# Performance work log

Hardware: AMD Instinct MI355X
Metric: run time of the kernel (lower is better)

## Reference

```python
import jax, jax.numpy as jnp
import numpy as np

D_MODEL, HEAD_DIM = 1024, 128

def setup_inputs() -> dict:
    key = jax.random.key(0)
    kx, kq, kk, kv = jax.random.split(key, 4)
    x = jax.random.normal(kx, (4, 4096, D_MODEL), dtype=jnp.float32)
    s = 1.0 / np.sqrt(D_MODEL)
    Wq = jax.random.normal(kq, (D_MODEL, HEAD_DIM), dtype=jnp.float32) * s
    Wk = jax.random.normal(kk, (D_MODEL, HEAD_DIM), dtype=jnp.float32) * s
    Wv = jax.random.normal(kv, (D_MODEL, HEAD_DIM), dtype=jnp.float32) * s
    return {"x": x, "Wq": Wq, "Wk": Wk, "Wv": Wv}

def reference(x, Wq, Wk, Wv):
    # x: [b, s, d_model]; Wq/Wk/Wv: [d_model, head_dim]
    q = jnp.einsum('bsd,dh->bsh', x, Wq)
    k = jnp.einsum('bsd,dh->bsh', x, Wk)
    v = jnp.einsum('bsd,dh->bsh', x, Wv)
    seq = x.shape[1]
    scale = 1.0 / jnp.sqrt(jnp.asarray(q.shape[-1], q.dtype))
    scores = jnp.einsum('bqh,bkh->bqk', q, k) * scale  # [b, s, s]
    causal = jnp.tril(jnp.ones((seq, seq), dtype=bool))
    scores = jnp.where(causal, scores, jnp.asarray(-jnp.inf, scores.dtype))
    attn = jax.nn.softmax(scores, axis=-1)
    return jnp.einsum('bqk,bkh->bqh', attn, v)
```

## Files before the change

kernel.cpp:

```cpp
#include <hip/hip_runtime.h>
#include <hip/hip_bf16.h>
#include <math.h>

#define D_MODEL 1024
#define HD 128
#define SEQ 4096

typedef __bf16 bf16x8 __attribute__((ext_vector_type(8)));
typedef float f32x4 __attribute__((ext_vector_type(4)));
typedef unsigned int u32;
typedef u32 u32x4 __attribute__((ext_vector_type(4)));

__device__ __forceinline__ unsigned short f2bf(float f) {
    union { float f; u32 u; } c; c.f = f;
    u32 u = c.u;
    u = (u + 0x7fffu + ((u >> 16) & 1u)) >> 16;
    return (unsigned short)u;
}
__device__ __forceinline__ u32 pk2(float a, float b) {
    __hip_bfloat162 h = __float22bfloat162_rn(make_float2(a, b));
    union { __hip_bfloat162 h; u32 u; } c; c.h = h; return c.u;
}
__device__ __forceinline__ void dma16(void* lds, const void* g) {
    __builtin_amdgcn_global_load_lds(
        (const __attribute__((address_space(1))) u32*)g,
        (__attribute__((address_space(3))) u32*)lds, 16, 0, 0);
}
__device__ __forceinline__ void drain_dma()  { __builtin_amdgcn_s_waitcnt(0x0F70); }
__device__ __forceinline__ void drain_dma4() { __builtin_amdgcn_s_waitcnt(0x0F74); }

__global__ __launch_bounds__(256)
void wt_kernel(const float* __restrict__ Wq, const float* __restrict__ Wk,
               const float* __restrict__ Wv, unsigned short* __restrict__ Wt) {
    __shared__ float wsf[64][129];
    const int t = threadIdx.x;
    const int k0 = blockIdx.x * 64;
    const int mat = blockIdx.y;
    const float* W = (mat == 0) ? Wq : (mat == 1) ? Wk : Wv;
    const float sc = (mat == 0) ? (0.08838834764831845f * 1.4426950408889634f) : 1.0f;
    {
        const int r = t >> 2, c = (t & 3) * 32;
        const float* src = W + (size_t)(k0 + r) * HD + c;
        #pragma unroll
        for (int j = 0; j < 32; j += 4)
            *reinterpret_cast<f32x4*>(&wsf[r][c + j]) = *reinterpret_cast<const f32x4*>(src + j);
    }
    __syncthreads();
    const int n = t >> 1, ks = (t & 1) * 32;
    u32 ow[16];
    #pragma unroll
    for (int j = 0; j < 16; ++j)
        ow[j] = pk2(wsf[ks + 2 * j][n] * sc, wsf[ks + 2 * j + 1][n] * sc);
    unsigned short* dst = Wt + (size_t)(mat * HD + n) * D_MODEL + k0 + ks;
    #pragma unroll
    for (int j = 0; j < 4; ++j)
        *reinterpret_cast<u32x4*>(dst + j * 8) = (u32x4){ow[4*j], ow[4*j+1], ow[4*j+2], ow[4*j+3]};
}

__global__ __launch_bounds__(256)
void proj_kernel(const float* __restrict__ x, const unsigned short* __restrict__ Wt,
                 unsigned short* __restrict__ Qb, unsigned short* __restrict__ Kb,
                 unsigned short* __restrict__ Vt) {
    __shared__ __align__(1024) char ps[49152];
    const int t = threadIdx.x;
    const int w = t >> 6, l = t & 63, li = l & 15, g2 = l >> 4;
    const int id = blockIdx.x;
    const int grp = id / 24, win = id % 24;
    const int nbase = (win >> 3) * 128;
    const int rowbase = (grp * 8 + (win & 7)) * 64;

    f32x4 acc[8];
    #pragma unroll
    for (int nt = 0; nt < 8; ++nt) acc[nt] = (f32x4){0.f, 0.f, 0.f, 0.f};

    const int lrow = l >> 3;
    const int xg = (l & 7) ^ (lrow & 6);
    const int wgr = (l & 7) ^ lrow;
    const int wrow_add = (wgr >> 2) << 6;
    const int wkc = (wgr & 3) * 8;

    auto stage = [&](int k0, int buf) {
        #pragma unroll
        for (int j = 0; j < 2; ++j) {
            int r0 = w * 16 + 8 * j;
            dma16(ps + buf * 8192 + r0 * 128,
                  x + (size_t)(rowbase + r0 + lrow) * D_MODEL + k0 + xg * 4);
            dma16(ps + 24576 + buf * 8192 + r0 * 128,
                  Wt + (size_t)(nbase + r0 + lrow + wrow_add) * D_MODEL + k0 + wkc);
        }
    };

    stage(0, 0);
    stage(32, 1);
    for (int it = 0; it < 32; ++it) {
        const int buf = it % 3;
        if (it < 31) drain_dma4(); else drain_dma();
        __syncthreads();
        if (it + 2 < 32) stage((it + 2) * 32, (it + 2) % 3);
        const char* xb = ps + buf * 8192 + (w * 16 + li) * 128 + (((2 * g2) ^ (li & 6)) * 16);
        f32x4 x0 = *reinterpret_cast<const f32x4*>(xb);
        f32x4 x1 = *reinterpret_cast<const f32x4*>(xb + 16);
        union { u32 d[4]; bf16x8 v; } cva;
        cva.d[0] = pk2(x0[0], x0[1]); cva.d[1] = pk2(x0[2], x0[3]);
        cva.d[2] = pk2(x1[0], x1[1]); cva.d[3] = pk2(x1[2], x1[3]);
        bf16x8 af = cva.v;
        #pragma unroll
        for (int nt = 0; nt < 8; ++nt) {
            bf16x8 bfr = *reinterpret_cast<const bf16x8*>(
                ps + 24576 + buf * 8192 + ((nt & 3) * 16 + li) * 128 +
                ((((nt >> 2) * 4 + g2) ^ (li & 7)) * 16));
            acc[nt] = __builtin_amdgcn_mfma_f32_16x16x32_bf16(af, bfr, acc[nt], 0, 0, 0);
        }
    }

    if (nbase < 256) {
        unsigned short* P = nbase ? Kb : Qb;
        #pragma unroll
        for (int nt = 0; nt < 8; ++nt)
            #pragma unroll
            for (int r = 0; r < 4; ++r) {
                int grow = rowbase + w * 16 + g2 * 4 + r;
                P[(size_t)grow * HD + nt * 16 + li] = f2bf(acc[nt][r]);
            }
    } else {
        int grow0 = rowbase + w * 16 + g2 * 4;
        int b_ = grow0 >> 12, s_ = grow0 & 4095;
        #pragma unroll
        for (int nt = 0; nt < 8; ++nt) {
            ushort4 s4;
            s4.x = f2bf(acc[nt][0]); s4.y = f2bf(acc[nt][1]);
            s4.z = f2bf(acc[nt][2]); s4.w = f2bf(acc[nt][3]);
            *reinterpret_cast<ushort4*>(&Vt[((size_t)b_ * HD + nt * 16 + li) * SEQ + s_]) = s4;
        }
    }
}

__global__ __launch_bounds__(256, 2)
void attn_kernel(const unsigned short* __restrict__ Qb, const unsigned short* __restrict__ Kb,
                 const unsigned short* __restrict__ Vt, float* __restrict__ outO,
                 unsigned short* __restrict__ Obf, float* __restrict__ Lbuf) {
    __shared__ __align__(1024) char smem[73728];
    const int t = threadIdx.x;
    const int w = t >> 6, l = t & 63, li = l & 15, g2 = l >> 4;
    const int qh = w >> 1, kh = w & 1;
    const int b = blockIdx.x & 3;
    const int u = blockIdx.x >> 2;
    const int g = 63 - (u >> 2);
    const int c = u & 3;
    const int R = g + 1;
    const int ts = (c * R) >> 2, te = ((c + 1) * R) >> 2;
    const int q0 = g * 64;
    const size_t rowb = (size_t)b * SEQ;
    const int koff = kh * 32;

    const unsigned short* KbB = Kb + rowb * HD;
    const unsigned short* VtB = Vt + (size_t)b * HD * SEQ;
    const int vgran = ((l & 7) ^ (l >> 3)) * 8;

    auto stage = [&](int it, char* base) {
        const int j0 = it * 64;
        #pragma unroll
        for (int j = 0; j < 4; ++j) {
            int rK = w * 16 + 4 * j + (l >> 4);
            dma16(base + (w * 16 + 4 * j) * 256,
                  KbB + (size_t)(j0 + rK) * 128 + (((l & 15) ^ (rK & 7)) * 8));
            int rV = w * 32 + 8 * j + (l >> 3);
            dma16(base + 16384 + (w * 32 + 8 * j) * 128,
                  VtB + (size_t)rV * SEQ + j0 + vgran);
        }
    };

    bf16x8 qf[2][4];
    #pragma unroll
    for (int qt = 0; qt < 2; ++qt)
        #pragma unroll
        for (int ks = 0; ks < 4; ++ks)
            qf[qt][ks] = *reinterpret_cast<const bf16x8*>(
                Qb + (rowb + q0 + qh * 32 + qt * 16 + li) * HD + ks * 32 + g2 * 8);

    f32x4 acco[2][8];
    #pragma unroll
    for (int qt = 0; qt < 2; ++qt)
        #pragma unroll
        for (int dt = 0; dt < 8; ++dt) acco[qt][dt] = (f32x4){0.f, 0.f, 0.f, 0.f};
    float ls[2] = {0.f, 0.f};

    const int gV = ((4 * kh + g2) ^ (li & 7)) * 16;

    if (ts < te) stage(ts, smem);
    for (int it = ts; it < te; ++it) {
        char* cbuf = smem + ((it - ts) & 1) * 32768;
        char* nbuf = smem + (((it - ts) & 1) ^ 1) * 32768;
        drain_dma();
        __syncthreads();
        if (it + 1 < te) stage(it + 1, nbuf);

        f32x4 accs[2][2];
        #pragma unroll
        for (int qt = 0; qt < 2; ++qt)
            #pragma unroll
            for (int kt = 0; kt < 2; ++kt) accs[qt][kt] = (f32x4){0.f, 0.f, 0.f, 0.f};
        #pragma unroll
        for (int kt = 0; kt < 2; ++kt) {
            const char* kb = cbuf + (koff + kt * 16 + li) * 256;
            #pragma unroll
            for (int ks = 0; ks < 4; ++ks) {
                bf16x8 kf = *reinterpret_cast<const bf16x8*>(kb + (((4 * ks + g2) ^ (li & 7)) * 16));
                accs[0][kt] = __builtin_amdgcn_mfma_f32_16x16x32_bf16(kf, qf[0][ks], accs[0][kt], 0, 0, 0);
                accs[1][kt] = __builtin_amdgcn_mfma_f32_16x16x32_bf16(kf, qf[1][ks], accs[1][kt], 0, 0, 0);
            }
        }

        const bool masked = (it == g);
        #pragma unroll
        for (int qt = 0; qt < 2; ++qt) {
            const int prow = qh * 32 + qt * 16 + li;
            #pragma unroll
            for (int kt = 0; kt < 2; ++kt) {
                float p[4];
                #pragma unroll
                for (int r = 0; r < 4; ++r) {
                    float s = accs[qt][kt][r];
                    if (masked && (koff + kt * 16 + g2 * 4 + r > prow)) s = -INFINITY;
                    p[r] = __builtin_amdgcn_exp2f(s - 16.0f);
                    ls[qt] += p[r];
                }
                union { u32 d[2]; uint2 v; } pw;
                pw.d[0] = pk2(p[0], p[1]); pw.d[1] = pk2(p[2], p[3]);
                int gr = (kh * 4 + kt * 2 + (g2 >> 1)) ^ (prow & 7);
                *reinterpret_cast<uint2*>(
                    smem + 65536 + prow * 128 + gr * 16 + (g2 & 1) * 8) = pw.v;
            }
        }

        bf16x8 pb[2];
        #pragma unroll
        for (int qt = 0; qt < 2; ++qt) {
            const int prow = qh * 32 + qt * 16 + li;
            pb[qt] = *reinterpret_cast<const bf16x8*>(
                smem + 65536 + prow * 128 + (((kh * 4 + g2) ^ (prow & 7)) * 16));
        }
        #pragma unroll
        for (int dt = 0; dt < 8; ++dt) {
            bf16x8 va = *reinterpret_cast<const bf16x8*>(cbuf + 16384 + (dt * 16 + li) * 128 + gV);
            acco[0][dt] = __builtin_amdgcn_mfma_f32_16x16x32_bf16(va, pb[0], acco[0][dt], 0, 0, 0);
            acco[1][dt] = __builtin_amdgcn_mfma_f32_16x16x32_bf16(va, pb[1], acco[1][dt], 0, 0, 0);
        }
    }

    #pragma unroll
    for (int qt = 0; qt < 2; ++qt) {
        ls[qt] += __shfl_xor(ls[qt], 16);
        ls[qt] += __shfl_xor(ls[qt], 32);
    }

    float (*Osum)[132] = (float(*)[132])smem;
    float* Lsh = (float*)(smem + 33792);
    __syncthreads();
    if (l < 16) {
        Lsh[kh * 64 + qh * 32 + l]      = ls[0];
        Lsh[kh * 64 + qh * 32 + 16 + l] = ls[1];
    }
    if (kh == 0) {
        #pragma unroll
        for (int qt = 0; qt < 2; ++qt)
            #pragma unroll
            for (int dt = 0; dt < 8; ++dt)
                *reinterpret_cast<f32x4*>(
                    &Osum[qh * 32 + qt * 16 + li][dt * 16 + g2 * 4]) = acco[qt][dt];
    }
    __syncthreads();
    if (kh == 1) {
        #pragma unroll
        for (int qt = 0; qt < 2; ++qt)
            #pragma unroll
            for (int dt = 0; dt < 8; ++dt) {
                f32x4* p = reinterpret_cast<f32x4*>(
                    &Osum[qh * 32 + qt * 16 + li][dt * 16 + g2 * 4]);
                f32x4 v = *p;
                #pragma unroll
                for (int j = 0; j < 4; ++j) v[j] += acco[qt][dt][j];
                *p = v;
            }
    }
    __syncthreads();

    if (t < 64)
        Lbuf[(size_t)c * 16384 + rowb + q0 + t] = Lsh[t] + Lsh[64 + t];
    #pragma unroll
    for (int k = 0; k < 8; ++k) {
        int idx = t + k * 256;
        int row = idx >> 5, col = (idx & 31) * 4;
        f32x4 o = *reinterpret_cast<const f32x4*>(&Osum[row][col]);
        size_t grow = rowb + q0 + row;
        if (c == 3) {
            *reinterpret_cast<f32x4*>(&outO[grow * HD + col]) = o;
        } else {
            union { u32 d[2]; uint2 v; } pkd;
            pkd.d[0] = pk2(o[0], o[1]); pkd.d[1] = pk2(o[2], o[3]);
            *reinterpret_cast<uint2*>(&Obf[(size_t)c * 2097152 + grow * HD + col]) = pkd.v;
        }
    }
}

__global__ __launch_bounds__(256)
void merge_kernel(float* __restrict__ outO, const unsigned short* __restrict__ Obf,
                  const float* __restrict__ Lbuf) {
    int tid = blockIdx.x * 256 + threadIdx.x;
    #pragma unroll
    for (int k = 0; k < 4; ++k) {
        int idx = tid + k * 131072;
        int row = idx >> 5, col = (idx & 31) * 4;
        float lsum = Lbuf[row] + Lbuf[16384 + row] + Lbuf[32768 + row] + Lbuf[49152 + row];
        float inv = 1.f / lsum;
        f32x4 o = *reinterpret_cast<const f32x4*>(&outO[(size_t)row * HD + col]);
        #pragma unroll
        for (int cc = 0; cc < 3; ++cc) {
            ushort4 uu = *reinterpret_cast<const ushort4*>(
                &Obf[(size_t)cc * 2097152 + (size_t)row * HD + col]);
            union { u32 u; float f; } a, b2, c2, d2;
            a.u = (u32)uu.x << 16; b2.u = (u32)uu.y << 16;
            c2.u = (u32)uu.z << 16; d2.u = (u32)uu.w << 16;
            o[0] += a.f; o[1] += b2.f; o[2] += c2.f; o[3] += d2.f;
        }
        #pragma unroll
        for (int j = 0; j < 4; ++j) o[j] *= inv;
        *reinterpret_cast<f32x4*>(&outO[(size_t)row * HD + col]) = o;
    }
}

extern "C" void kernel_launch(void* const* d_in, const int* in_sizes, int n_in,
                              void* d_out, int out_size, void* d_ws, size_t ws_size,
                              hipStream_t stream) {
    const float* x  = (const float*)d_in[0];
    const float* Wq = (const float*)d_in[1];
    const float* Wk = (const float*)d_in[2];
    const float* Wv = (const float*)d_in[3];
    float* out = (float*)d_out;

    char* ws = (char*)d_ws;
    unsigned short* Qb  = (unsigned short*)(ws);
    unsigned short* Kb  = (unsigned short*)(ws + ((size_t)4  << 20));
    unsigned short* Vt  = (unsigned short*)(ws + ((size_t)8  << 20));
    unsigned short* Wt  = (unsigned short*)(ws + ((size_t)12 << 20));
    unsigned short* Obf = (unsigned short*)(ws + ((size_t)13 << 20));
    float*          Lb  = (float*)(ws + ((size_t)25 << 20));

    wt_kernel   <<<dim3(16, 3), dim3(256), 0, stream>>>(Wq, Wk, Wv, Wt);
    proj_kernel <<<dim3(768),   dim3(256), 0, stream>>>(x, Wt, Qb, Kb, Vt);
    attn_kernel <<<dim3(1024),  dim3(256), 0, stream>>>(Qb, Kb, Vt, out, Obf, Lb);
    merge_kernel<<<dim3(512),   dim3(256), 0, stream>>>(out, Obf, Lb);
}
```

Baseline: 167.1 us.

## Replace LDS-staged projection pipeline with direct global-to-register double buffering

The projection kernel no longer stages x and W tiles through LDS with async DMA and barriers. Each lane now loads its A and B fragments straight from global memory into registers, using a two-stage register double buffer, and the launch bounds ask for 3 blocks per SM. This removes the LDS round trip and the __syncthreads per k-step. In exchange there is no data sharing across waves: every wave re-reads the W fragments from global/L2, and register pressure goes up.

Result: slower. 235.8 us (+41.1%).

```diff
diff --git a/kernel.cpp b/kernel.cpp
--- a/kernel.cpp
+++ b/kernel.cpp
@@ -27,7 +27,6 @@
         (__attribute__((address_space(3))) u32*)lds, 16, 0, 0);
 }
 __device__ __forceinline__ void drain_dma()  { __builtin_amdgcn_s_waitcnt(0x0F70); }
-__device__ __forceinline__ void drain_dma4() { __builtin_amdgcn_s_waitcnt(0x0F74); }
 
 __global__ __launch_bounds__(256)
 void wt_kernel(const float* __restrict__ Wq, const float* __restrict__ Wk,
@@ -57,11 +56,30 @@
         *reinterpret_cast<u32x4*>(dst + j * 8) = (u32x4){ow[4*j], ow[4*j+1], ow[4*j+2], ow[4*j+3]};
 }
 
-__global__ __launch_bounds__(256)
+struct PStage { f32x4 a0, a1; bf16x8 b[8]; };
+
+__device__ __forceinline__ void ld_stage(PStage& S, const float* xq,
+                                         const unsigned short* wq) {
+    S.a0 = *reinterpret_cast<const f32x4*>(xq);
+    S.a1 = *reinterpret_cast<const f32x4*>(xq + 4);
+    #pragma unroll
+    for (int nt = 0; nt < 8; ++nt)
+        S.b[nt] = *reinterpret_cast<const bf16x8*>(wq + nt * 16 * D_MODEL);
+}
+__device__ __forceinline__ void do_stage(const PStage& S, f32x4* acc) {
+    union { u32 d[4]; bf16x8 v; } cva;
+    cva.d[0] = pk2(S.a0[0], S.a0[1]); cva.d[1] = pk2(S.a0[2], S.a0[3]);
+    cva.d[2] = pk2(S.a1[0], S.a1[1]); cva.d[3] = pk2(S.a1[2], S.a1[3]);
+    bf16x8 af = cva.v;
+    #pragma unroll
+    for (int nt = 0; nt < 8; ++nt)
+        acc[nt] = __builtin_amdgcn_mfma_f32_16x16x32_bf16(af, S.b[nt], acc[nt], 0, 0, 0);
+}
+
+__global__ __launch_bounds__(256, 3)
 void proj_kernel(const float* __restrict__ x, const unsigned short* __restrict__ Wt,
                  unsigned short* __restrict__ Qb, unsigned short* __restrict__ Kb,
                  unsigned short* __restrict__ Vt) {
-    __shared__ __align__(1024) char ps[49152];
     const int t = threadIdx.x;
     const int w = t >> 6, l = t & 63, li = l & 15, g2 = l >> 4;
     const int id = blockIdx.x;
@@ -69,49 +87,26 @@
     const int nbase = (win >> 3) * 128;
     const int rowbase = (grp * 8 + (win & 7)) * 64;
 
+    const float* xq = x + (size_t)(rowbase + w * 16 + li) * D_MODEL + g2 * 8;
+    const unsigned short* wq = Wt + (size_t)(nbase + li) * D_MODEL + g2 * 8;
+
     f32x4 acc[8];
     #pragma unroll
     for (int nt = 0; nt < 8; ++nt) acc[nt] = (f32x4){0.f, 0.f, 0.f, 0.f};
 
-    const int lrow = l >> 3;
-    const int xg = (l & 7) ^ (lrow & 6);
-    const int wgr = (l & 7) ^ lrow;
-    const int wrow_add = (wgr >> 2) << 6;
-    const int wkc = (wgr & 3) * 8;
-
-    auto stage = [&](int k0, int buf) {
-        #pragma unroll
-        for (int j = 0; j < 2; ++j) {
-            int r0 = w * 16 + 8 * j;
-            dma16(ps + buf * 8192 + r0 * 128,
-                  x + (size_t)(rowbase + r0 + lrow) * D_MODEL + k0 + xg * 4);
-            dma16(ps + 24576 + buf * 8192 + r0 * 128,
-                  Wt + (size_t)(nbase + r0 + lrow + wrow_add) * D_MODEL + k0 + wkc);
-        }
-    };
-
-    stage(0, 0);
-    stage(32, 1);
-    for (int it = 0; it < 32; ++it) {
-        const int buf = it % 3;
-        if (it < 31) drain_dma4(); else drain_dma();
-        __syncthreads();
-        if (it + 2 < 32) stage((it + 2) * 32, (it + 2) % 3);
-        const char* xb = ps + buf * 8192 + (w * 16 + li) * 128 + (((2 * g2) ^ (li & 6)) * 16);
-        f32x4 x0 = *reinterpret_cast<const f32x4*>(xb);
-        f32x4 x1 = *reinterpret_cast<const f32x4*>(xb + 16);
-        union { u32 d[4]; bf16x8 v; } cva;
-        cva.d[0] = pk2(x0[0], x0[1]); cva.d[1] = pk2(x0[2], x0[3]);
-        cva.d[2] = pk2(x1[0], x1[1]); cva.d[3] = pk2(x1[2], x1[3]);
-        bf16x8 af = cva.v;
-        #pragma unroll
-        for (int nt = 0; nt < 8; ++nt) {
-            bf16x8 bfr = *reinterpret_cast<const bf16x8*>(
-                ps + 24576 + buf * 8192 + ((nt & 3) * 16 + li) * 128 +
-                ((((nt >> 2) * 4 + g2) ^ (li & 7)) * 16));
-            acc[nt] = __builtin_amdgcn_mfma_f32_16x16x32_bf16(af, bfr, acc[nt], 0, 0, 0);
-        }
-    }
+    PStage S0, S1;
+    ld_stage(S0, xq, wq);
+    ld_stage(S1, xq + 32, wq + 32);
+
+    for (int it = 0; it < 30; it += 2) {
+        do_stage(S0, acc);
+        ld_stage(S0, xq + 64, wq + 64);
+        do_stage(S1, acc);
+        ld_stage(S1, xq + 96, wq + 96);
+        xq += 64; wq += 64;
+    }
+    do_stage(S0, acc);
+    do_stage(S1, acc);
 
     if (nbase < 256) {
         unsigned short* P = nbase ? Kb : Qb;
```

## Compute Q, K and V together per row tile in projection kernel

Applied to the files above, without the earlier changes.

The projection kernel now uses 512-thread blocks that each compute a 64-row tile against all 384 Q/K/V output columns. Before, three separate blocks computed the three projections and each re-read the same fp32 x rows, so x is now fetched once instead of three times. The software pipeline deepens from 3 to 4 LDS stages, and each wave computes a 2x6 MFMA tile with B fragments reused across the M subtiles. The cost is 128KB of LDS per block, which limits occupancy to one block per CU and gives only 256 blocks for the whole grid.

New measurement: 168.1 us. No clear change (+0.6%).

```diff
diff --git a/kernel.cpp b/kernel.cpp
--- a/kernel.cpp
+++ b/kernel.cpp
@@ -27,7 +27,6 @@
         (__attribute__((address_space(3))) u32*)lds, 16, 0, 0);
 }
 __device__ __forceinline__ void drain_dma()  { __builtin_amdgcn_s_waitcnt(0x0F70); }
-__device__ __forceinline__ void drain_dma4() { __builtin_amdgcn_s_waitcnt(0x0F74); }
 
 __global__ __launch_bounds__(256)
 void wt_kernel(const float* __restrict__ Wq, const float* __restrict__ Wk,
@@ -57,80 +56,94 @@
         *reinterpret_cast<u32x4*>(dst + j * 8) = (u32x4){ow[4*j], ow[4*j+1], ow[4*j+2], ow[4*j+3]};
 }
 
-__global__ __launch_bounds__(256)
+__global__ __launch_bounds__(512, 2)
 void proj_kernel(const float* __restrict__ x, const unsigned short* __restrict__ Wt,
                  unsigned short* __restrict__ Qb, unsigned short* __restrict__ Kb,
                  unsigned short* __restrict__ Vt) {
-    __shared__ __align__(1024) char ps[49152];
+    __shared__ __align__(1024) char ps[131072];
     const int t = threadIdx.x;
     const int w = t >> 6, l = t & 63, li = l & 15, g2 = l >> 4;
-    const int id = blockIdx.x;
-    const int grp = id / 24, win = id % 24;
-    const int nbase = (win >> 3) * 128;
-    const int rowbase = (grp * 8 + (win & 7)) * 64;
-
-    f32x4 acc[8];
-    #pragma unroll
-    for (int nt = 0; nt < 8; ++nt) acc[nt] = (f32x4){0.f, 0.f, 0.f, 0.f};
-
-    const int lrow = l >> 3;
-    const int xg = (l & 7) ^ (lrow & 6);
-    const int wgr = (l & 7) ^ lrow;
-    const int wrow_add = (wgr >> 2) << 6;
-    const int wkc = (wgr & 3) * 8;
-
-    auto stage = [&](int k0, int buf) {
-        #pragma unroll
-        for (int j = 0; j < 2; ++j) {
-            int r0 = w * 16 + 8 * j;
-            dma16(ps + buf * 8192 + r0 * 128,
-                  x + (size_t)(rowbase + r0 + lrow) * D_MODEL + k0 + xg * 4);
-            dma16(ps + 24576 + buf * 8192 + r0 * 128,
-                  Wt + (size_t)(nbase + r0 + lrow + wrow_add) * D_MODEL + k0 + wkc);
+    const int mh = w >> 2, nq = w & 3;
+    const int rowbase = blockIdx.x * 64;
+
+    const int lr = l >> 3, lg = l & 7;
+    const int cg = lg ^ lr;
+    const int wn_add = (cg >> 2) * 192;
+    const int wkq = (cg & 3) * 8;
+
+    auto stage = [&](int it) {
+        const int k0 = it * 32;
+        const int buf = it & 3;
+        dma16(ps + buf * 8192 + w * 1024,
+              x + (size_t)(rowbase + w * 8 + lr) * D_MODEL + k0 + cg * 4);
+        #pragma unroll
+        for (int j = 0; j < 3; ++j) {
+            int r0 = w * 24 + j * 8;
+            dma16(ps + 32768 + buf * 24576 + r0 * 128,
+                  Wt + (size_t)(r0 + lr + wn_add) * D_MODEL + k0 + wkq);
         }
     };
 
-    stage(0, 0);
-    stage(32, 1);
+    f32x4 acc[2][6];
+    #pragma unroll
+    for (int mt = 0; mt < 2; ++mt)
+        #pragma unroll
+        for (int nt = 0; nt < 6; ++nt) acc[mt][nt] = (f32x4){0.f, 0.f, 0.f, 0.f};
+
+    stage(0); stage(1); stage(2);
     for (int it = 0; it < 32; ++it) {
-        const int buf = it % 3;
-        if (it < 31) drain_dma4(); else drain_dma();
+        if (it < 30)       __builtin_amdgcn_s_waitcnt(0x0F78);
+        else if (it == 30) __builtin_amdgcn_s_waitcnt(0x0F74);
+        else               drain_dma();
         __syncthreads();
-        if (it + 2 < 32) stage((it + 2) * 32, (it + 2) % 3);
-        const char* xb = ps + buf * 8192 + (w * 16 + li) * 128 + (((2 * g2) ^ (li & 6)) * 16);
-        f32x4 x0 = *reinterpret_cast<const f32x4*>(xb);
-        f32x4 x1 = *reinterpret_cast<const f32x4*>(xb + 16);
-        union { u32 d[4]; bf16x8 v; } cva;
-        cva.d[0] = pk2(x0[0], x0[1]); cva.d[1] = pk2(x0[2], x0[3]);
-        cva.d[2] = pk2(x1[0], x1[1]); cva.d[3] = pk2(x1[2], x1[3]);
-        bf16x8 af = cva.v;
-        #pragma unroll
-        for (int nt = 0; nt < 8; ++nt) {
-            bf16x8 bfr = *reinterpret_cast<const bf16x8*>(
-                ps + 24576 + buf * 8192 + ((nt & 3) * 16 + li) * 128 +
-                ((((nt >> 2) * 4 + g2) ^ (li & 7)) * 16));
-            acc[nt] = __builtin_amdgcn_mfma_f32_16x16x32_bf16(af, bfr, acc[nt], 0, 0, 0);
-        }
-    }
-
-    if (nbase < 256) {
-        unsigned short* P = nbase ? Kb : Qb;
-        #pragma unroll
-        for (int nt = 0; nt < 8; ++nt)
-            #pragma unroll
-            for (int r = 0; r < 4; ++r) {
-                int grow = rowbase + w * 16 + g2 * 4 + r;
-                P[(size_t)grow * HD + nt * 16 + li] = f2bf(acc[nt][r]);
+        if (it + 3 < 32) stage(it + 3);
+
+        const char* xb = ps + (it & 3) * 8192;
+        const char* wb = ps + 32768 + (it & 3) * 24576;
+
+        bf16x8 bf[6];
+        #pragma unroll
+        for (int nt = 0; nt < 6; ++nt) {
+            int r = (nq & 1) * 96 + nt * 16 + li;
+            bf[nt] = *reinterpret_cast<const bf16x8*>(
+                wb + r * 128 + ((((nq >> 1) * 4 + g2) ^ (li & 7)) * 16));
+        }
+        #pragma unroll
+        for (int mt = 0; mt < 2; ++mt) {
+            int row = mh * 32 + mt * 16 + li;
+            int p0 = ((2 * g2) ^ (li & 7)) * 16;
+            f32x4 x0 = *reinterpret_cast<const f32x4*>(xb + row * 128 + p0);
+            f32x4 x1 = *reinterpret_cast<const f32x4*>(xb + row * 128 + (p0 ^ 16));
+            union { u32 d[4]; bf16x8 v; } cva;
+            cva.d[0] = pk2(x0[0], x0[1]); cva.d[1] = pk2(x0[2], x0[3]);
+            cva.d[2] = pk2(x1[0], x1[1]); cva.d[3] = pk2(x1[2], x1[3]);
+            bf16x8 af = cva.v;
+            #pragma unroll
+            for (int nt = 0; nt < 6; ++nt)
+                acc[mt][nt] = __builtin_amdgcn_mfma_f32_16x16x32_bf16(af, bf[nt], acc[mt][nt], 0, 0, 0);
+        }
+    }
+
+    #pragma unroll
+    for (int nt = 0; nt < 6; ++nt) {
+        const int c0 = nq * 96 + nt * 16;
+        #pragma unroll
+        for (int mt = 0; mt < 2; ++mt) {
+            const int m0 = mh * 32 + mt * 16 + g2 * 4;
+            if (c0 < 256) {
+                unsigned short* P = (c0 < 128) ? Qb : Kb;
+                const int col = (c0 < 128 ? c0 : c0 - 128) + li;
+                #pragma unroll
+                for (int r = 0; r < 4; ++r)
+                    P[(size_t)(rowbase + m0 + r) * HD + col] = f2bf(acc[mt][nt][r]);
+            } else {
+                const int d = c0 - 256 + li;
+                const int b_ = rowbase >> 12, s_ = (rowbase + m0) & 4095;
+                ushort4 s4;
+                s4.x = f2bf(acc[mt][nt][0]); s4.y = f2bf(acc[mt][nt][1]);
+                s4.z = f2bf(acc[mt][nt][2]); s4.w = f2bf(acc[mt][nt][3]);
+                *reinterpret_cast<ushort4*>(&Vt[((size_t)b_ * HD + d) * SEQ + s_]) = s4;
             }
-    } else {
-        int grow0 = rowbase + w * 16 + g2 * 4;
-        int b_ = grow0 >> 12, s_ = grow0 & 4095;
-        #pragma unroll
-        for (int nt = 0; nt < 8; ++nt) {
-            ushort4 s4;
-            s4.x = f2bf(acc[nt][0]); s4.y = f2bf(acc[nt][1]);
-            s4.z = f2bf(acc[nt][2]); s4.w = f2bf(acc[nt][3]);
-            *reinterpret_cast<ushort4*>(&Vt[((size_t)b_ * HD + nt * 16 + li) * SEQ + s_]) = s4;
         }
     }
 }
@@ -347,7 +360,7 @@
     float*          Lb  = (float*)(ws + ((size_t)25 << 20));
 
     wt_kernel   <<<dim3(16, 3), dim3(256), 0, stream>>>(Wq, Wk, Wv, Wt);
-    proj_kernel <<<dim3(768),   dim3(256), 0, stream>>>(x, Wt, Qb, Kb, Vt);
+    proj_kernel <<<dim3(256),   dim3(512), 0, stream>>>(x, Wt, Qb, Kb, Vt);
     attn_kernel <<<dim3(1024),  dim3(256), 0, stream>>>(Qb, Kb, Vt, out, Obf, Lb);
     merge_kernel<<<dim3(512),   dim3(256), 0, stream>>>(out, Obf, Lb);
 }
```
